# Kernel optimization log

Measured on AMD Instinct MI355X. Metric: run time of the kernel, lower is better.

## Reference

```python
import jax, jax.numpy as jnp
from jax import lax
import numpy as np

SEQ_LEN, BATCH, X_DIM = 512, 128, 256
PHI, R, OUT = 512, 256, 256
ALPHAS = (0.0, 0.5, 0.9, 0.99)
MU = PHI * len(ALPHAS)


def setup_inputs() -> dict:
    key = jax.random.key(0)
    ks = jax.random.split(key, 4)
    s = 0.02  # xavier-ish scale for stability
    return {
        "inputs": jax.random.normal(ks[0], (SEQ_LEN, BATCH, X_DIM), jnp.float32),
        "W_mu2r": jax.random.normal(ks[1], (R, MU), jnp.float32) * s,
        "b_mu2r": jnp.zeros((R,), jnp.float32),
        "W_xr2phi": jax.random.normal(ks[2], (PHI, X_DIM + R), jnp.float32) * s,
        "b_xr2phi": jnp.zeros((PHI,), jnp.float32),
        "W_mu2o": jax.random.normal(ks[3], (OUT, MU), jnp.float32) * s,
        "b_mu2o": jnp.zeros((OUT,), jnp.float32),
    }


def reference(inputs, W_mu2r, b_mu2r, W_xr2phi, b_xr2phi, W_mu2o, b_mu2o):
    A = jnp.asarray(ALPHAS, dtype=inputs.dtype)          # (n_alpha,) non-trainable buffer
    n_alpha = A.shape[0]
    phi_size = W_xr2phi.shape[0]
    # A_mask = kron(A, ones(1, phi)) -> each alpha repeated phi_size times: (1, mu)
    a_mask = jnp.repeat(A, phi_size)[None, :]

    def step(mu, x):
        r = jax.nn.relu(mu @ W_mu2r.T + b_mu2r)                             # (B, r)
        phi = jax.nn.relu(jnp.concatenate([x, r], axis=1) @ W_xr2phi.T + b_xr2phi)  # (B, phi)
        phi_tile = jnp.tile(phi, (1, n_alpha))                              # kron(ones, phi): (B, mu)
        mu = a_mask * mu + (1.0 - a_mask) * phi_tile
        return mu, None

    mu0 = jnp.zeros((inputs.shape[1], phi_size * n_alpha), inputs.dtype)
    mu, _ = lax.scan(step, mu0, inputs)
    return jax.nn.relu(mu @ W_mu2o.T + b_mu2o)  # (B, out)
```

## Files before the change

kernel.cpp:

```cpp
#include <hip/hip_runtime.h>
#include <hip/hip_bf16.h>

#define SEQ   512
#define BATCH 128
#define XD    256
#define PHID  512
#define RD    256
#define OUTD  256
#define NBLK  48
#define RING  16

typedef __attribute__((ext_vector_type(8))) short short8;
typedef __attribute__((ext_vector_type(4))) float floatx4;

#define MFMA(a, b, c) __builtin_amdgcn_mfma_f32_16x16x32_bf16((a), (b), (c), 0, 0, 0)

#define WAITVM(N) do { asm volatile("s_waitcnt vmcnt(" #N ")" ::: "memory"); \
                       __builtin_amdgcn_sched_barrier(0); } while (0)

#define SPIN(P, TGT) do { int _it = 0; \
    while (flagld(P) < (TGT)) { if (++_it > 32768) break; } } while (0)

__device__ inline short8 ldg8(const __hip_bfloat16* p) {
    return *reinterpret_cast<const short8*>(p);
}
__device__ inline void ldcc(short8& d, const __hip_bfloat16* p) {
    asm volatile("global_load_dwordx4 %0, %1, off sc1"
                 : "=v"(d) : "v"(p) : "memory");
}
__device__ inline void stcc16(__hip_bfloat16* p, __hip_bfloat16 v) {
    const short sv = __builtin_bit_cast(short, v);
    asm volatile("global_store_short %0, %1, off sc1"
                 :: "v"(p), "v"(sv) : "memory");
}
__device__ inline int flagld(const int* p) {
    return __hip_atomic_load(p, __ATOMIC_RELAXED, __HIP_MEMORY_SCOPE_AGENT);
}
__device__ inline void flag_sc1(int* p, int v) {
    asm volatile("global_store_dword %0, %1, off sc1"
                 :: "v"(p), "v"(v) : "memory");
}

__global__ void convert_x(const float* __restrict__ x, __hip_bfloat16* __restrict__ xbf) {
    const int gid = blockIdx.x * blockDim.x + threadIdx.x;
    const float4 v = reinterpret_cast<const float4*>(x)[gid];
    __hip_bfloat16* d = xbf + 4 * (size_t)gid;
    d[0] = __float2bfloat16(v.x); d[1] = __float2bfloat16(v.y);
    d[2] = __float2bfloat16(v.z); d[3] = __float2bfloat16(v.w);
}

__global__ void __launch_bounds__(256) sru_pipe(
    const float* __restrict__ W1, const float* __restrict__ W2,
    const float* __restrict__ Wo,
    const float* __restrict__ b1, const float* __restrict__ b2,
    const float* __restrict__ bo,
    const __hip_bfloat16* __restrict__ xbf,
    __hip_bfloat16* __restrict__ rbf,
    __hip_bfloat16* __restrict__ phib,
    float* __restrict__ out, int* __restrict__ ctrl)
{
    __shared__ __hip_bfloat16 wlds[32768];
    const int bid  = blockIdx.x;
    const int tid  = threadIdx.x;
    const int wave = tid >> 6;
    const int lane = tid & 63;
    const int quad = lane >> 4;
    const int lrow = lane & 15;
    const int m0   = wave * 32;
    int* rfl = ctrl;
    int* pfl = ctrl + 256;
    int* ofl = ctrl + 512;

    if (bid < 16) {
        const int j0 = bid * 32;
        for (int i = tid * 4; i < 2 * 32 * 256; i += 1024) {
            const int part = i >> 13, rem = i & 8191;
            const int n = rem >> 8, k = rem & 255;
            const float4 v = *reinterpret_cast<const float4*>(
                &W2[(j0 + n) * (XD + RD) + part * 256 + k]);
            __hip_bfloat16* dst = &wlds[(((part * 32 + (k >> 3)) * 32 + n) << 3) + (k & 7)];
            dst[0] = __float2bfloat16(v.x); dst[1] = __float2bfloat16(v.y);
            dst[2] = __float2bfloat16(v.z); dst[3] = __float2bfloat16(v.w);
        }
        __syncthreads();
        const float bj0 = b2[j0 + lrow];
        const float bj1 = b2[j0 + 16 + lrow];
        const __hip_bfloat16* rb0 = rbf + (m0 + lrow) * RD + 8 * quad;
        const __hip_bfloat16* rb1 = rbf + (m0 + 16 + lrow) * RD + 8 * quad;
        #pragma unroll 1
        for (int t = 0; t < SEQ; ++t) {
            floatx4 acc[2][2] = {};
            const __hip_bfloat16* xt = xbf + (size_t)(t * BATCH + m0) * XD;
            #pragma unroll
            for (int k = 0; k < XD; k += 32) {
                const short8 a0 = ldg8(xt + lrow * XD + k + 8 * quad);
                const short8 a1 = ldg8(xt + (16 + lrow) * XD + k + 8 * quad);
                #pragma unroll
                for (int j2 = 0; j2 < 2; ++j2) {
                    const short8 b = *reinterpret_cast<const short8*>(
                        &wlds[((((k >> 3) + quad) * 32 + j2 * 16 + lrow) << 3)]);
                    acc[0][j2] = MFMA(a0, b, acc[0][j2]);
                    acc[1][j2] = MFMA(a1, b, acc[1][j2]);
                }
            }
            if (tid < 16) {
                SPIN(&rfl[tid * 16], t + 1);
            } else if (tid < 32) {
                SPIN(&ofl[(tid - 16) * 16], t - 15);
            }
            __syncthreads();
            short8 ra[2][4][2];
            #pragma unroll
            for (int ki = 0; ki < 4; ++ki) {
                ldcc(ra[0][ki][0], rb0 + ki * 32);
                ldcc(ra[0][ki][1], rb1 + ki * 32);
            }
            #pragma unroll
            for (int g = 0; g < 2; ++g) {
                if (g == 0) {
                    #pragma unroll
                    for (int ki = 0; ki < 4; ++ki) {
                        ldcc(ra[1][ki][0], rb0 + 128 + ki * 32);
                        ldcc(ra[1][ki][1], rb1 + 128 + ki * 32);
                    }
                    WAITVM(8);
                } else {
                    WAITVM(0);
                }
                #pragma unroll
                for (int ki = 0; ki < 4; ++ki) {
                    const int k = g * 128 + ki * 32;
                    #pragma unroll
                    for (int j2 = 0; j2 < 2; ++j2) {
                        const short8 b = *reinterpret_cast<const short8*>(
                            &wlds[(((32 + (k >> 3) + quad) * 32 + j2 * 16 + lrow) << 3)]);
                        acc[0][j2] = MFMA(ra[g][ki][0], b, acc[0][j2]);
                        acc[1][j2] = MFMA(ra[g][ki][1], b, acc[1][j2]);
                    }
                }
            }
            __hip_bfloat16* pb = phib + (size_t)(t & (RING - 1)) * BATCH * PHID;
            #pragma unroll
            for (int h = 0; h < 2; ++h)
                #pragma unroll
                for (int j2 = 0; j2 < 2; ++j2)
                    #pragma unroll
                    for (int i = 0; i < 4; ++i) {
                        const int row = m0 + 16 * h + quad * 4 + i;
                        const float v = acc[h][j2][i] + (j2 ? bj1 : bj0);
                        stcc16(pb + row * PHID + j0 + j2 * 16 + lrow,
                               __float2bfloat16(fmaxf(v, 0.f)));
                    }
            asm volatile("s_waitcnt vmcnt(0)" ::: "memory");
            __syncthreads();
            if (tid == 0) flag_sc1(&pfl[bid * 16], t + 1);
        }
    } else if (bid < 32) {
        const int sb = bid - 16, j0 = sb * 16;
        for (int i = tid * 4; i < 4 * 16 * 512; i += 1024) {
            const int a = i >> 13, rem = i & 8191;
            const int n = rem >> 9, k = rem & 511;
            const float4 v = *reinterpret_cast<const float4*>(
                &W1[(j0 + n) * 2048 + a * 512 + k]);
            __hip_bfloat16* dst = &wlds[(((a * 64 + (k >> 3)) * 16 + n) << 3) + (k & 7)];
            dst[0] = __float2bfloat16(v.x); dst[1] = __float2bfloat16(v.y);
            dst[2] = __float2bfloat16(v.z); dst[3] = __float2bfloat16(v.w);
        }
        __syncthreads();
        const float bjv = b1[j0 + lrow];
        const float pre[4]  = {0.f, 1.f, 9.f, 99.f};
        const float post[4] = {1.f, 0.5f, 0.1f, 0.01f};
        floatx4 s[4][2] = {};
        #pragma unroll 1
        for (int t = 0; t < SEQ; ++t) {
            #pragma unroll
            for (int h = 0; h < 2; ++h)
                #pragma unroll
                for (int i = 0; i < 4; ++i) {
                    const int row = m0 + 16 * h + quad * 4 + i;
                    const float rv = s[0][h][i] + s[1][h][i] + s[2][h][i] + s[3][h][i] + bjv;
                    stcc16(rbf + row * RD + j0 + lrow, __float2bfloat16(fmaxf(rv, 0.f)));
                }
            asm volatile("s_waitcnt vmcnt(0)" ::: "memory");
            __syncthreads();
            if (tid == 0) flag_sc1(&rfl[sb * 16], t + 1);
            if (t == SEQ - 1) break;
            if (tid < 16) {
                SPIN(&pfl[tid * 16], t + 1);
            }
            __syncthreads();
            #pragma unroll
            for (int a = 0; a < 4; ++a)
                #pragma unroll
                for (int h = 0; h < 2; ++h)
                    s[a][h] *= pre[a];
            const __hip_bfloat16* pb = phib + (size_t)(t & (RING - 1)) * BATCH * PHID;
            const __hip_bfloat16* pb0 = pb + (m0 + lrow) * PHID + 8 * quad;
            const __hip_bfloat16* pb1 = pb + (m0 + 16 + lrow) * PHID + 8 * quad;
            short8 fa[2][4][2];
            #pragma unroll
            for (int ki = 0; ki < 4; ++ki) {
                ldcc(fa[0][ki][0], pb0 + ki * 32);
                ldcc(fa[0][ki][1], pb1 + ki * 32);
            }
            #pragma unroll
            for (int g = 0; g < 4; ++g) {
                if (g < 3) {
                    #pragma unroll
                    for (int ki = 0; ki < 4; ++ki) {
                        ldcc(fa[(g + 1) & 1][ki][0], pb0 + (g + 1) * 128 + ki * 32);
                        ldcc(fa[(g + 1) & 1][ki][1], pb1 + (g + 1) * 128 + ki * 32);
                    }
                    WAITVM(8);
                } else {
                    WAITVM(0);
                }
                #pragma unroll
                for (int ki = 0; ki < 4; ++ki) {
                    const int k = g * 128 + ki * 32;
                    #pragma unroll
                    for (int a = 0; a < 4; ++a) {
                        const short8 b = *reinterpret_cast<const short8*>(
                            &wlds[(((a * 64 + (k >> 3) + quad) * 16 + lrow) << 3)]);
                        s[a][0] = MFMA(fa[g & 1][ki][0], b, s[a][0]);
                        s[a][1] = MFMA(fa[g & 1][ki][1], b, s[a][1]);
                    }
                }
            }
            #pragma unroll
            for (int a = 0; a < 4; ++a)
                #pragma unroll
                for (int h = 0; h < 2; ++h)
                    s[a][h] *= post[a];
        }
    } else {
        const int ob = bid - 32, j0 = ob * 16;
        for (int i = tid * 4; i < 4 * 16 * 512; i += 1024) {
            const int a = i >> 13, rem = i & 8191;
            const int n = rem >> 9, k = rem & 511;
            const float4 v = *reinterpret_cast<const float4*>(
                &Wo[(j0 + n) * 2048 + a * 512 + k]);
            __hip_bfloat16* dst = &wlds[(((a * 64 + (k >> 3)) * 16 + n) << 3) + (k & 7)];
            dst[0] = __float2bfloat16(v.x); dst[1] = __float2bfloat16(v.y);
            dst[2] = __float2bfloat16(v.z); dst[3] = __float2bfloat16(v.w);
        }
        __syncthreads();
        const float pre[4]  = {0.f, 1.f, 9.f, 99.f};
        const float post[4] = {1.f, 0.5f, 0.1f, 0.01f};
        floatx4 o[4][2] = {};
        #pragma unroll 1
        for (int t = 0; t < SEQ; ++t) {
            if (tid < 16) {
                SPIN(&pfl[tid * 16], t + 1);
            }
            __syncthreads();
            #pragma unroll
            for (int a = 0; a < 4; ++a)
                #pragma unroll
                for (int h = 0; h < 2; ++h)
                    o[a][h] *= pre[a];
            const __hip_bfloat16* pb = phib + (size_t)(t & (RING - 1)) * BATCH * PHID;
            const __hip_bfloat16* pb0 = pb + (m0 + lrow) * PHID + 8 * quad;
            const __hip_bfloat16* pb1 = pb + (m0 + 16 + lrow) * PHID + 8 * quad;
            short8 fa[2][4][2];
            #pragma unroll
            for (int ki = 0; ki < 4; ++ki) {
                ldcc(fa[0][ki][0], pb0 + ki * 32);
                ldcc(fa[0][ki][1], pb1 + ki * 32);
            }
            #pragma unroll
            for (int g = 0; g < 4; ++g) {
                if (g < 3) {
                    #pragma unroll
                    for (int ki = 0; ki < 4; ++ki) {
                        ldcc(fa[(g + 1) & 1][ki][0], pb0 + (g + 1) * 128 + ki * 32);
                        ldcc(fa[(g + 1) & 1][ki][1], pb1 + (g + 1) * 128 + ki * 32);
                    }
                    WAITVM(8);
                } else {
                    WAITVM(0);
                }
                #pragma unroll
                for (int ki = 0; ki < 4; ++ki) {
                    const int k = g * 128 + ki * 32;
                    #pragma unroll
                    for (int a = 0; a < 4; ++a) {
                        const short8 b = *reinterpret_cast<const short8*>(
                            &wlds[(((a * 64 + (k >> 3) + quad) * 16 + lrow) << 3)]);
                        o[a][0] = MFMA(fa[g & 1][ki][0], b, o[a][0]);
                        o[a][1] = MFMA(fa[g & 1][ki][1], b, o[a][1]);
                    }
                }
            }
            #pragma unroll
            for (int a = 0; a < 4; ++a)
                #pragma unroll
                for (int h = 0; h < 2; ++h)
                    o[a][h] *= post[a];
            __syncthreads();
            if (tid == 0) flag_sc1(&ofl[ob * 16], t + 1);
        }
        const float bjo = bo[j0 + lrow];
        #pragma unroll
        for (int h = 0; h < 2; ++h)
            #pragma unroll
            for (int i = 0; i < 4; ++i) {
                const int row = m0 + 16 * h + quad * 4 + i;
                const float v = o[0][h][i] + o[1][h][i] + o[2][h][i] + o[3][h][i] + bjo;
                out[row * OUTD + j0 + lrow] = fmaxf(v, 0.f);
            }
    }
}

extern "C" void kernel_launch(void* const* d_in, const int* in_sizes, int n_in,
                              void* d_out, int out_size, void* d_ws, size_t ws_size,
                              hipStream_t stream)
{
    const float* x  = (const float*)d_in[0];
    const float* W1 = (const float*)d_in[1];
    const float* b1 = (const float*)d_in[2];
    const float* W2 = (const float*)d_in[3];
    const float* b2 = (const float*)d_in[4];
    const float* Wo = (const float*)d_in[5];
    const float* bo = (const float*)d_in[6];
    float* out = (float*)d_out;
    char* ws = (char*)d_ws;

    constexpr size_t O_CTRL = 0;
    constexpr size_t O_RBF  = 4096;
    constexpr size_t O_PHI  = O_RBF + (size_t)BATCH * RD * 2;
    constexpr size_t O_X    = O_PHI + (size_t)RING * BATCH * PHID * 2;

    hipMemsetAsync(ws + O_CTRL, 0, 3072, stream);
    convert_x<<<SEQ * BATCH * XD / 4 / 256, 256, 0, stream>>>(
        x, (__hip_bfloat16*)(ws + O_X));
    sru_pipe<<<NBLK, 256, 0, stream>>>(
        W1, W2, Wo, b1, b2, bo,
        (const __hip_bfloat16*)(ws + O_X),
        (__hip_bfloat16*)(ws + O_RBF),
        (__hip_bfloat16*)(ws + O_PHI),
        out, (int*)(ws + O_CTRL));
}
```

Baseline: 4.854 ms.

## Switch to per-wave flags and halve phi blocks with wider tiles

```diff
diff --git a/kernel.cpp b/kernel.cpp
--- a/kernel.cpp
+++ b/kernel.cpp
@@ -7,7 +7,10 @@
 #define PHID  512
 #define RD    256
 #define OUTD  256
-#define NBLK  48
+#define NPHI  8
+#define NS    16
+#define NO    16
+#define NBLK  (NPHI + NS + NO)
 #define RING  16
 
 typedef __attribute__((ext_vector_type(8))) short short8;
@@ -17,9 +20,6 @@
 
 #define WAITVM(N) do { asm volatile("s_waitcnt vmcnt(" #N ")" ::: "memory"); \
                        __builtin_amdgcn_sched_barrier(0); } while (0)
-
-#define SPIN(P, TGT) do { int _it = 0; \
-    while (flagld(P) < (TGT)) { if (++_it > 32768) break; } } while (0)
 
 __device__ inline short8 ldg8(const __hip_bfloat16* p) {
     return *reinterpret_cast<const short8*>(p);
@@ -68,47 +68,51 @@
     const int lrow = lane & 15;
     const int m0   = wave * 32;
     int* rfl = ctrl;
-    int* pfl = ctrl + 256;
-    int* ofl = ctrl + 512;
-
-    if (bid < 16) {
-        const int j0 = bid * 32;
-        for (int i = tid * 4; i < 2 * 32 * 256; i += 1024) {
-            const int part = i >> 13, rem = i & 8191;
-            const int n = rem >> 8, k = rem & 255;
-            const float4 v = *reinterpret_cast<const float4*>(
-                &W2[(j0 + n) * (XD + RD) + part * 256 + k]);
-            __hip_bfloat16* dst = &wlds[(((part * 32 + (k >> 3)) * 32 + n) << 3) + (k & 7)];
+    int* pfl = ctrl + 1024;
+    int* ofl = ctrl + 1536;
+
+    if (bid < NPHI) {
+        const int j0 = bid * 64;
+        for (int i = tid * 4; i < 64 * 512; i += 1024) {
+            const int n = i >> 9, k = i & 511;
+            const int part = k >> 8, kk = k & 255;
+            const float4 v = *reinterpret_cast<const float4*>(&W2[(j0 + n) * 512 + k]);
+            __hip_bfloat16* dst = &wlds[(((part * 32 + (kk >> 3)) * 64 + n) << 3) + (kk & 7)];
             dst[0] = __float2bfloat16(v.x); dst[1] = __float2bfloat16(v.y);
             dst[2] = __float2bfloat16(v.z); dst[3] = __float2bfloat16(v.w);
         }
         __syncthreads();
-        const float bj0 = b2[j0 + lrow];
-        const float bj1 = b2[j0 + 16 + lrow];
+        float bj[4];
+        #pragma unroll
+        for (int j2 = 0; j2 < 4; ++j2) bj[j2] = b2[j0 + j2 * 16 + lrow];
         const __hip_bfloat16* rb0 = rbf + (m0 + lrow) * RD + 8 * quad;
         const __hip_bfloat16* rb1 = rbf + (m0 + 16 + lrow) * RD + 8 * quad;
         #pragma unroll 1
         for (int t = 0; t < SEQ; ++t) {
-            floatx4 acc[2][2] = {};
+            floatx4 acc[2][4] = {};
             const __hip_bfloat16* xt = xbf + (size_t)(t * BATCH + m0) * XD;
             #pragma unroll
             for (int k = 0; k < XD; k += 32) {
                 const short8 a0 = ldg8(xt + lrow * XD + k + 8 * quad);
                 const short8 a1 = ldg8(xt + (16 + lrow) * XD + k + 8 * quad);
                 #pragma unroll
-                for (int j2 = 0; j2 < 2; ++j2) {
+                for (int j2 = 0; j2 < 4; ++j2) {
                     const short8 b = *reinterpret_cast<const short8*>(
-                        &wlds[((((k >> 3) + quad) * 32 + j2 * 16 + lrow) << 3)]);
+                        &wlds[((((k >> 3) + quad) * 64 + j2 * 16 + lrow) << 3)]);
                     acc[0][j2] = MFMA(a0, b, acc[0][j2]);
                     acc[1][j2] = MFMA(a1, b, acc[1][j2]);
                 }
             }
-            if (tid < 16) {
-                SPIN(&rfl[tid * 16], t + 1);
-            } else if (tid < 32) {
-                SPIN(&ofl[(tid - 16) * 16], t - 15);
-            }
-            __syncthreads();
+            {
+                int guard = 0;
+                while (true) {
+                    bool nr = false;
+                    if (lane < 16)      nr = flagld(&rfl[(lane * 4 + wave) * 16]) < t + 1;
+                    else if (lane < 32) nr = flagld(&ofl[((lane - 16) * 4 + wave) * 16]) < t - (RING - 1);
+                    if (__ballot(nr) == 0) break;
+                    if (++guard > 16384) break;
+                }
+            }
             short8 ra[2][4][2];
             #pragma unroll
             for (int ki = 0; ki < 4; ++ki) {
@@ -131,9 +135,9 @@
                 for (int ki = 0; ki < 4; ++ki) {
                     const int k = g * 128 + ki * 32;
                     #pragma unroll
-                    for (int j2 = 0; j2 < 2; ++j2) {
+                    for (int j2 = 0; j2 < 4; ++j2) {
                         const short8 b = *reinterpret_cast<const short8*>(
-                            &wlds[(((32 + (k >> 3) + quad) * 32 + j2 * 16 + lrow) << 3)]);
+                            &wlds[(((32 + (k >> 3) + quad) * 64 + j2 * 16 + lrow) << 3)]);
                         acc[0][j2] = MFMA(ra[g][ki][0], b, acc[0][j2]);
                         acc[1][j2] = MFMA(ra[g][ki][1], b, acc[1][j2]);
                     }
@@ -143,20 +147,19 @@
             #pragma unroll
             for (int h = 0; h < 2; ++h)
                 #pragma unroll
-                for (int j2 = 0; j2 < 2; ++j2)
+                for (int j2 = 0; j2 < 4; ++j2)
                     #pragma unroll
                     for (int i = 0; i < 4; ++i) {
                         const int row = m0 + 16 * h + quad * 4 + i;
-                        const float v = acc[h][j2][i] + (j2 ? bj1 : bj0);
+                        const float v = acc[h][j2][i] + bj[j2];
                         stcc16(pb + row * PHID + j0 + j2 * 16 + lrow,
                                __float2bfloat16(fmaxf(v, 0.f)));
                     }
             asm volatile("s_waitcnt vmcnt(0)" ::: "memory");
-            __syncthreads();
-            if (tid == 0) flag_sc1(&pfl[bid * 16], t + 1);
-        }
-    } else if (bid < 32) {
-        const int sb = bid - 16, j0 = sb * 16;
+            if (lane == 0) flag_sc1(&pfl[(bid * 4 + wave) * 16], t + 1);
+        }
+    } else if (bid < NPHI + NS) {
+        const int sb = bid - NPHI, j0 = sb * 16;
         for (int i = tid * 4; i < 4 * 16 * 512; i += 1024) {
             const int a = i >> 13, rem = i & 8191;
             const int n = rem >> 9, k = rem & 511;
@@ -182,13 +185,17 @@
                     stcc16(rbf + row * RD + j0 + lrow, __float2bfloat16(fmaxf(rv, 0.f)));
                 }
             asm volatile("s_waitcnt vmcnt(0)" ::: "memory");
-            __syncthreads();
-            if (tid == 0) flag_sc1(&rfl[sb * 16], t + 1);
+            if (lane == 0) flag_sc1(&rfl[(sb * 4 + wave) * 16], t + 1);
             if (t == SEQ - 1) break;
-            if (tid < 16) {
-                SPIN(&pfl[tid * 16], t + 1);
-            }
-            __syncthreads();
+            {
+                int guard = 0;
+                while (true) {
+                    bool nr = false;
+                    if (lane < 8) nr = flagld(&pfl[(lane * 4 + wave) * 16]) < t + 1;
+                    if (__ballot(nr) == 0) break;
+                    if (++guard > 16384) break;
+                }
+            }
             #pragma unroll
             for (int a = 0; a < 4; ++a)
                 #pragma unroll
@@ -234,7 +241,7 @@
                     s[a][h] *= post[a];
         }
     } else {
-        const int ob = bid - 32, j0 = ob * 16;
+        const int ob = bid - NPHI - NS, j0 = ob * 16;
         for (int i = tid * 4; i < 4 * 16 * 512; i += 1024) {
             const int a = i >> 13, rem = i & 8191;
             const int n = rem >> 9, k = rem & 511;
@@ -250,10 +257,15 @@
         floatx4 o[4][2] = {};
         #pragma unroll 1
         for (int t = 0; t < SEQ; ++t) {
-            if (tid < 16) {
-                SPIN(&pfl[tid * 16], t + 1);
-            }
-            __syncthreads();
+            {
+                int guard = 0;
+                while (true) {
+                    bool nr = false;
+                    if (lane < 8) nr = flagld(&pfl[(lane * 4 + wave) * 16]) < t + 1;
+                    if (__ballot(nr) == 0) break;
+                    if (++guard > 16384) break;
+                }
+            }
             #pragma unroll
             for (int a = 0; a < 4; ++a)
                 #pragma unroll
@@ -297,8 +309,7 @@
                 #pragma unroll
                 for (int h = 0; h < 2; ++h)
                     o[a][h] *= post[a];
-            __syncthreads();
-            if (tid == 0) flag_sc1(&ofl[ob * 16], t + 1);
+            if (lane == 0) flag_sc1(&ofl[(ob * 4 + wave) * 16], t + 1);
         }
         const float bjo = bo[j0 + lrow];
         #pragma unroll
@@ -327,11 +338,11 @@
     char* ws = (char*)d_ws;
 
     constexpr size_t O_CTRL = 0;
-    constexpr size_t O_RBF  = 4096;
+    constexpr size_t O_RBF  = 16384;
     constexpr size_t O_PHI  = O_RBF + (size_t)BATCH * RD * 2;
     constexpr size_t O_X    = O_PHI + (size_t)RING * BATCH * PHID * 2;
 
-    hipMemsetAsync(ws + O_CTRL, 0, 3072, stream);
+    hipMemsetAsync(ws + O_CTRL, 0, 12288, stream);
     convert_x<<<SEQ * BATCH * XD / 4 / 256, 256, 0, stream>>>(
         x, (__hip_bfloat16*)(ws + O_X));
     sru_pipe<<<NBLK, 256, 0, stream>>>(
```

Result: faster. 4.219 ms (-13.1%).
